# Performance work log

Measured on AMD Instinct MI355X. Metric: run time of the kernel, lower is better.

The kernel has to match this reference:

```python
import jax, jax.numpy as jnp
import numpy as np

N, E, D, L = 50000, 400000, 128, 5
NTYPE, NATTR, NDEPTH = 100, 100, 21
BN_EPS = 1e-5


def _bn(z, gamma, beta):
    # training-mode BatchNorm1d over the node axis (biased variance, as torch)
    mu = jnp.mean(z, axis=0)
    var = jnp.mean(jnp.square(z - mu), axis=0)
    return (z - mu) * jax.lax.rsqrt(var + BN_EPS) * gamma + beta


def setup_inputs() -> dict:
    key = jax.random.key(0)
    ks = jax.random.split(key, 20)
    s = 0.05
    inp = {
        "x": jax.random.randint(ks[0], (N, 2), 0, NTYPE),
        "node_depth": jax.random.randint(ks[1], (N,), 0, NDEPTH),
        "edge_index": jax.random.randint(ks[2], (2, E), 0, N),
        "edge_attr": jax.random.normal(ks[3], (E, 2), dtype=jnp.float32),
        # node encoder tables
        "type_emb": jax.random.normal(ks[4], (NTYPE, D)) * s,
        "attr_emb": jax.random.normal(ks[5], (NATTR, D)) * s,
        "depth_emb": jax.random.normal(ks[6], (NDEPTH, D)) * s,
        # per-layer GIN params, stacked over L
        "We": jax.random.normal(ks[7], (L, 2, D)) * s,
        "be": jnp.zeros((L, D)),
        "eps": jnp.zeros((L,)),
        "W1": jax.random.normal(ks[8], (L, D, 2 * D)) * s,
        "b1": jnp.zeros((L, 2 * D)),
        "g1": jnp.ones((L, 2 * D)),
        "bt1": jnp.zeros((L, 2 * D)),
        "W2": jax.random.normal(ks[9], (L, 2 * D, D)) * s,
        "b2": jnp.zeros((L, D)),
        "go": jnp.ones((L, D)),
        "bo": jnp.zeros((L, D)),
    }
    return inp


def reference(x, node_depth, edge_index, edge_attr,
              type_emb, attr_emb, depth_emb,
              We, be, eps, W1, b1, g1, bt1, W2, b2, go, bo):
    # node encoder: type + attr + depth embeddings  -> [N, D]
    h = (type_emb[x[:, 0]] + attr_emb[x[:, 1]]
         + depth_emb[jnp.clip(node_depth, 0, NDEPTH - 1)])
    src, dst = edge_index[0], edge_index[1]
    n = h.shape[0]
    for l in range(L):
        # GINConv: gather -> relu(x_j + edge_emb) -> scatter-add
        edge_emb = edge_attr @ We[l] + be[l]                 # [E, D]
        msg = jax.nn.relu(h[src] + edge_emb)                 # [E, D]
        agg = jax.ops.segment_sum(msg, dst, num_segments=n)  # [N, D]
        z = (1.0 + eps[l]) * h + agg
        # mlp: Linear -> BN -> ReLU -> Linear
        z = _bn(z @ W1[l] + b1[l], g1[l], bt1[l])
        z = jax.nn.relu(z) @ W2[l] + b2[l]
        # outer batchnorm
        z = _bn(z, go[l], bo[l])
        if l < L - 1:  # relu on all but last layer (dropout p=0 -> identity)
            z = jax.nn.relu(z)
        h = z
    return h  # JK='last'
```

## Files before the change

kernel.cpp:

```cpp
#include <hip/hip_runtime.h>
#include <hip/hip_bf16.h>

#define NN  50000
#define NE  400000
#define DD  128
#define DD2 256
#define NL  5
#define NB_SCAN 196
#define GB  256
#define NCH 1563

typedef __hip_bfloat16 bf16;
typedef __attribute__((ext_vector_type(8))) short bf16x8;
typedef __attribute__((ext_vector_type(4))) float f32x4;

__device__ __forceinline__ float b2f(bf16 v) { return __bfloat162float(v); }
__device__ __forceinline__ bool probe_bf(const void* g1) {
    return ((const unsigned*)g1)[0] == 0x3F803F80u;
}
__device__ __forceinline__ float ldp(const void* p, int i, bool bf) {
    return bf ? b2f(((const bf16*)p)[i]) : ((const float*)p)[i];
}
__device__ __forceinline__ void ldp8(const void* p, int i, bool bf, float* o) {
    if (bf) {
        union { int4 v; bf16 b[8]; } u;
        u.v = *(const int4*)((const bf16*)p + i);
#pragma unroll
        for (int j = 0; j < 8; j++) o[j] = b2f(u.b[j]);
    } else {
        float4 a = *(const float4*)((const float*)p + i);
        float4 b = *(const float4*)((const float*)p + i + 4);
        o[0]=a.x; o[1]=a.y; o[2]=a.z; o[3]=a.w;
        o[4]=b.x; o[5]=b.y; o[6]=b.z; o[7]=b.w;
    }
}

__global__ void enc_kernel(const int* __restrict__ x, const int* __restrict__ dep,
                           const void* te, const void* ae, const void* de,
                           const void* probe, float* __restrict__ h,
                           bf16* __restrict__ h2, int h2ok) {
    int t = blockIdx.x * 256 + threadIdx.x;
    if (t >= NN * DD) return;
    bool bf = probe_bf(probe);
    int i = t >> 7, d = t & (DD - 1);
    int dp = dep[i];
    dp = dp < 0 ? 0 : (dp > 20 ? 20 : dp);
    float a = ldp(te, x[2 * i] * DD + d, bf);
    float b = ldp(ae, x[2 * i + 1] * DD + d, bf);
    float c = ldp(de, dp * DD + d, bf);
    float s;
    if (bf) {
        s = b2f(__float2bfloat16(a + b));
        s = b2f(__float2bfloat16(s + c));
    } else {
        s = a + b + c;
    }
    h[t] = s;
    if (h2ok) h2[t] = __float2bfloat16(s);
}

__global__ void hist_kernel(const int* __restrict__ ei, int* __restrict__ cnt) {
    int e = blockIdx.x * 256 + threadIdx.x;
    if (e < NE) atomicAdd(&cnt[ei[NE + e]], 1);
}

__global__ void bsum_kernel(const int* __restrict__ cnt, int* __restrict__ bsum) {
    __shared__ int sm[256];
    int i = blockIdx.x * 256 + threadIdx.x;
    sm[threadIdx.x] = (i < NN) ? cnt[i] : 0;
    __syncthreads();
    for (int s = 128; s > 0; s >>= 1) {
        if (threadIdx.x < s) sm[threadIdx.x] += sm[threadIdx.x + s];
        __syncthreads();
    }
    if (threadIdx.x == 0) bsum[blockIdx.x] = sm[0];
}

__global__ void bscan_kernel(const int* __restrict__ bsum, int* __restrict__ boff, int nb) {
    __shared__ int sm[256];
    int t = threadIdx.x;
    int v = (t < nb) ? bsum[t] : 0;
    sm[t] = v; __syncthreads();
    for (int s = 1; s < 256; s <<= 1) {
        int a = (t >= s) ? sm[t - s] : 0;
        __syncthreads();
        sm[t] += a;
        __syncthreads();
    }
    if (t < nb) boff[t] = sm[t] - v;
}

__global__ void offs_kernel(const int* __restrict__ cnt, const int* __restrict__ boff,
                            int* __restrict__ offs, int* __restrict__ cur) {
    __shared__ int sm[256];
    int t = threadIdx.x;
    int i = blockIdx.x * 256 + t;
    int v = (i < NN) ? cnt[i] : 0;
    sm[t] = v; __syncthreads();
    for (int s = 1; s < 256; s <<= 1) {
        int a = (t >= s) ? sm[t - s] : 0;
        __syncthreads();
        sm[t] += a;
        __syncthreads();
    }
    int excl = sm[t] - v + boff[blockIdx.x];
    if (i < NN) { offs[i] = excl; cur[i] = excl; }
    if (i == NN - 1) offs[NN] = excl + v;
}

__global__ void place_kernel(const int* __restrict__ ei, const float* __restrict__ ea,
                             int* __restrict__ cur, int* __restrict__ srcS,
                             unsigned* __restrict__ eaS) {
    int e = blockIdx.x * 256 + threadIdx.x;
    if (e >= NE) return;
    int dst = ei[NE + e];
    int p = atomicAdd(&cur[dst], 1);
    srcS[p] = ei[e];
    union { bf16 b[2]; unsigned u; } pk;
    pk.b[0] = __float2bfloat16(ea[2 * e]);
    pk.b[1] = __float2bfloat16(ea[2 * e + 1]);
    eaS[p] = pk.u;
}

__global__ void wtrans2_kernel(const void* W1, const void* W2, const void* probe,
                               bf16* __restrict__ W1tH, bf16* __restrict__ W1tL,
                               bf16* __restrict__ W2tH, bf16* __restrict__ W2tL) {
    bool bf = probe_bf(probe);
    int idx = blockIdx.x * 256 + threadIdx.x;
    if (idx >= NL * DD * DD2) return;
    int l = idx / (DD * DD2), rem = idx % (DD * DD2);
    {
        int k = rem / DD2, n = rem % DD2;
        float w = ldp(W1, idx, bf);
        bf16 hb = __float2bfloat16(w);
        size_t o = ((size_t)l * DD2 + n) * DD + k;
        W1tH[o] = hb;
        W1tL[o] = __float2bfloat16(w - b2f(hb));
    }
    {
        int k = rem / DD, n = rem % DD;
        float w = ldp(W2, idx, bf);
        bf16 hb = __float2bfloat16(w);
        size_t o = ((size_t)l * DD + n) * DD2 + k;
        W2tH[o] = hb;
        W2tL[o] = __float2bfloat16(w - b2f(hb));
    }
}

template<int H2, int FIRST>
__global__ __launch_bounds__(256)
void agg_v3(const int* __restrict__ offs, const int* __restrict__ srcS,
            const unsigned* __restrict__ eaS, const void* We, const void* be,
            const void* epsp, const void* probe, const float* __restrict__ zmid,
            const bf16* __restrict__ zmid2, const float* __restrict__ s2v,
            const float* __restrict__ t2v, float* __restrict__ aggout, int l) {
    bool bf = probe_bf(probe);
    int wave = threadIdx.x >> 6, lane = threadIdx.x & 63;
    int node = blockIdx.x * 4 + wave;
    if (node >= NN) return;
    int d0 = lane * 2;
    float w00 = ldp(We, l * 2 * DD + d0, bf),      w01 = ldp(We, l * 2 * DD + d0 + 1, bf);
    float w10 = ldp(We, l * 2 * DD + DD + d0, bf), w11 = ldp(We, l * 2 * DD + DD + d0 + 1, bf);
    float bb0 = ldp(be, l * DD + d0, bf),          bb1 = ldp(be, l * DD + d0 + 1, bf);
    float cf = 1.0f + ldp(epsp, l, bf);
    float s20 = 1.f, s21 = 1.f, t20 = 0.f, t21 = 0.f;
    if (!FIRST) {
        float2 sv = *(const float2*)&s2v[d0];
        float2 tv = *(const float2*)&t2v[d0];
        s20 = sv.x; s21 = sv.y; t20 = tv.x; t21 = tv.y;
    }
    int s = offs[node], e = offs[node + 1];
    float acc0 = 0.f, acc1 = 0.f;
    int j = s;
#define AGG_ONE(SRC, EA)                                                        \
    {   float hx, hy;                                                          \
        if (H2) { union { unsigned u; bf16 b[2]; } hv;                         \
                  hv.u = *(const unsigned*)&zmid2[(size_t)(SRC) * DD + d0];    \
                  hx = b2f(hv.b[0]); hy = b2f(hv.b[1]); }                      \
        else    { float2 hv = *(const float2*)&zmid[(size_t)(SRC) * DD + d0];  \
                  hx = hv.x; hy = hv.y; }                                      \
        if (!FIRST) {                                                          \
            hx = fmaxf(fmaf(hx, s20, t20), 0.f);                               \
            hy = fmaxf(fmaf(hy, s21, t21), 0.f);                               \
        }                                                                      \
        union { unsigned u; bf16 b[2]; } ap; ap.u = (EA);                      \
        float ax = b2f(ap.b[0]), ay = b2f(ap.b[1]);                            \
        acc0 += fmaxf(hx + ax * w00 + ay * w10 + bb0, 0.f);                    \
        acc1 += fmaxf(hy + ax * w01 + ay * w11 + bb1, 0.f); }
    for (; j + 8 <= e; j += 8) {
        int i0=srcS[j],i1=srcS[j+1],i2=srcS[j+2],i3=srcS[j+3];
        int i4=srcS[j+4],i5=srcS[j+5],i6=srcS[j+6],i7=srcS[j+7];
        unsigned e0=eaS[j],e1=eaS[j+1],e2=eaS[j+2],e3=eaS[j+3];
        unsigned e4=eaS[j+4],e5=eaS[j+5],e6=eaS[j+6],e7=eaS[j+7];
        AGG_ONE(i0,e0) AGG_ONE(i1,e1) AGG_ONE(i2,e2) AGG_ONE(i3,e3)
        AGG_ONE(i4,e4) AGG_ONE(i5,e5) AGG_ONE(i6,e6) AGG_ONE(i7,e7)
    }
    for (; j + 4 <= e; j += 4) {
        int i0=srcS[j],i1=srcS[j+1],i2=srcS[j+2],i3=srcS[j+3];
        unsigned e0=eaS[j],e1=eaS[j+1],e2=eaS[j+2],e3=eaS[j+3];
        AGG_ONE(i0,e0) AGG_ONE(i1,e1) AGG_ONE(i2,e2) AGG_ONE(i3,e3)
    }
    for (; j < e; j++) { int i0 = srcS[j]; unsigned e0 = eaS[j]; AGG_ONE(i0,e0) }
#undef AGG_ONE
    float2 zs = *(const float2*)&zmid[(size_t)node * DD + d0];
    float h0 = zs.x, h1 = zs.y;
    if (!FIRST) {
        h0 = fmaxf(fmaf(h0, s20, t20), 0.f);
        h1 = fmaxf(fmaf(h1, s21, t21), 0.f);
    }
    float2 o; o.x = fmaf(cf, h0, acc0); o.y = fmaf(cf, h1, acc1);
    *(float2*)&aggout[(size_t)node * DD + d0] = o;
}

__global__ __launch_bounds__(512, 2)
void gemm1_v2(const float* __restrict__ zpre, const bf16* __restrict__ W1tH,
              const bf16* __restrict__ W1tL, const void* b1, const void* probe,
              bf16* __restrict__ z1, float* __restrict__ P1s, float* __restrict__ P1q,
              int l) {
    __shared__ float smS[DD2], smQ[DD2];
    bool bf = probe_bf(probe);
    int tid = threadIdx.x;
    int lane = tid & 63, wave = tid >> 6;
    int wq = wave & 3, wr = wave >> 2;
    int ln15 = lane & 15, kg = lane >> 4;

    const bf16* WlH = W1tH + (size_t)l * DD2 * DD;
    const bf16* WlL = W1tL + (size_t)l * DD2 * DD;

    bf16x8 bh[4][4], bl[4][4];
#pragma unroll
    for (int t = 0; t < 4; t++) {
        int n = (wq * 4 + t) * 16 + ln15;
#pragma unroll
        for (int s = 0; s < 4; s++) {
            size_t off = (size_t)n * DD + s * 32 + kg * 8;
            bh[t][s] = *(const bf16x8*)&WlH[off];
            bl[t][s] = *(const bf16x8*)&WlL[off];
        }
    }
    float bias[4];
#pragma unroll
    for (int t = 0; t < 4; t++) bias[t] = ldp(b1, l * DD2 + (wq * 4 + t) * 16 + ln15, bf);

    float sp[4] = {0.f, 0.f, 0.f, 0.f}, qp[4] = {0.f, 0.f, 0.f, 0.f};

    for (int chunk = blockIdx.x; chunk < NCH; chunk += GB) {
        int rowbase = chunk * 32 + wr * 16;
        int arow = rowbase + ln15;
        bool aval = arow < NN;
        f32x4 acc[4];
#pragma unroll
        for (int t = 0; t < 4; t++) acc[t] = (f32x4){0.f, 0.f, 0.f, 0.f};
#pragma unroll
        for (int s = 0; s < 4; s++) {
            float av[8];
            if (aval) {
                float4 p0 = *(const float4*)&zpre[(size_t)arow * DD + s * 32 + kg * 8];
                float4 p1 = *(const float4*)&zpre[(size_t)arow * DD + s * 32 + kg * 8 + 4];
                av[0]=p0.x; av[1]=p0.y; av[2]=p0.z; av[3]=p0.w;
                av[4]=p1.x; av[5]=p1.y; av[6]=p1.z; av[7]=p1.w;
            } else {
#pragma unroll
                for (int j = 0; j < 8; j++) av[j] = 0.f;
            }
            union { bf16x8 v; bf16 e[8]; } ahi, alo;
#pragma unroll
            for (int j = 0; j < 8; j++) {
                bf16 hb = __float2bfloat16(av[j]);
                ahi.e[j] = hb;
                alo.e[j] = __float2bfloat16(av[j] - b2f(hb));
            }
#pragma unroll
            for (int t = 0; t < 4; t++) {
                acc[t] = __builtin_amdgcn_mfma_f32_16x16x32_bf16(ahi.v, bh[t][s], acc[t], 0, 0, 0);
                acc[t] = __builtin_amdgcn_mfma_f32_16x16x32_bf16(alo.v, bh[t][s], acc[t], 0, 0, 0);
                acc[t] = __builtin_amdgcn_mfma_f32_16x16x32_bf16(ahi.v, bl[t][s], acc[t], 0, 0, 0);
            }
        }
#pragma unroll
        for (int t = 0; t < 4; t++) {
            int col = (wq * 4 + t) * 16 + ln15;
#pragma unroll
            for (int r = 0; r < 4; r++) {
                int row = rowbase + kg * 4 + r;
                if (row < NN) {
                    float zv = acc[t][r] + bias[t];
                    bf16 zb = __float2bfloat16(zv);
                    z1[(size_t)row * DD2 + col] = zb;
                    float vv = b2f(zb);
                    sp[t] += vv; qp[t] += vv * vv;
                }
            }
        }
    }
#pragma unroll
    for (int t = 0; t < 4; t++) {
        sp[t] += __shfl_xor(sp[t], 16); sp[t] += __shfl_xor(sp[t], 32);
        qp[t] += __shfl_xor(qp[t], 16); qp[t] += __shfl_xor(qp[t], 32);
    }
    if (tid < DD2) { smS[tid] = 0.f; smQ[tid] = 0.f; }
    __syncthreads();
    if ((lane & 48) == 0) {
#pragma unroll
        for (int t = 0; t < 4; t++) {
            int col = (wq * 4 + t) * 16 + ln15;
            atomicAdd(&smS[col], sp[t]);
            atomicAdd(&smQ[col], qp[t]);
        }
    }
    __syncthreads();
    if (tid < DD2) {
        P1s[(size_t)blockIdx.x * DD2 + tid] = smS[tid];
        P1q[(size_t)blockIdx.x * DD2 + tid] = smQ[tid];
    }
}

__global__ __launch_bounds__(512, 2)
void gemm2_v2(const bf16* __restrict__ z1, const float* __restrict__ s1,
              const float* __restrict__ t1, const bf16* __restrict__ W2tH,
              const bf16* __restrict__ W2tL, const void* b2, const void* probe,
              float* __restrict__ out, bf16* __restrict__ out2, int shadow,
              float* __restrict__ P2s, float* __restrict__ P2q, int l) {
    __shared__ float smS[DD], smQ[DD];
    bool bf = probe_bf(probe);
    int tid = threadIdx.x;
    int lane = tid & 63, wave = tid >> 6;
    int wq = wave & 3, wr = wave >> 2;
    int ln15 = lane & 15, kg = lane >> 4;

    const bf16* WlH = W2tH + (size_t)l * DD * DD2;
    const bf16* WlL = W2tL + (size_t)l * DD * DD2;

    bf16x8 bh[2][8], bl[2][8];
#pragma unroll
    for (int t = 0; t < 2; t++) {
        int n = (wq * 2 + t) * 16 + ln15;
#pragma unroll
        for (int s = 0; s < 8; s++) {
            size_t off = (size_t)n * DD2 + s * 32 + kg * 8;
            bh[t][s] = *(const bf16x8*)&WlH[off];
            bl[t][s] = *(const bf16x8*)&WlL[off];
        }
    }
    float bias[2];
#pragma unroll
    for (int t = 0; t < 2; t++) bias[t] = ldp(b2, l * DD + (wq * 2 + t) * 16 + ln15, bf);

    float sp[2] = {0.f, 0.f}, qp[2] = {0.f, 0.f};

    for (int chunk = blockIdx.x; chunk < NCH; chunk += GB) {
        int rowbase = chunk * 32 + wr * 16;
        int arow = rowbase + ln15;
        bool aval = arow < NN;
        f32x4 acc[2];
        acc[0] = (f32x4){0.f, 0.f, 0.f, 0.f};
        acc[1] = (f32x4){0.f, 0.f, 0.f, 0.f};
#pragma unroll
        for (int s = 0; s < 8; s++) {
            int k0 = s * 32 + kg * 8;
            float az[8];
            if (aval) {
                union { int4 v; bf16 b[8]; } u;
                u.v = *(const int4*)&z1[(size_t)arow * DD2 + k0];
                float4 c0 = *(const float4*)&s1[k0];
                float4 c1 = *(const float4*)&s1[k0 + 4];
                float4 d0 = *(const float4*)&t1[k0];
                float4 d1 = *(const float4*)&t1[k0 + 4];
                float sc[8] = {c0.x,c0.y,c0.z,c0.w,c1.x,c1.y,c1.z,c1.w};
                float tt[8] = {d0.x,d0.y,d0.z,d0.w,d1.x,d1.y,d1.z,d1.w};
#pragma unroll
                for (int j = 0; j < 8; j++)
                    az[j] = fmaxf(fmaf(b2f(u.b[j]), sc[j], tt[j]), 0.f);
            } else {
#pragma unroll
                for (int j = 0; j < 8; j++) az[j] = 0.f;
            }
            union { bf16x8 v; bf16 e[8]; } ahi, alo;
#pragma unroll
            for (int j = 0; j < 8; j++) {
                bf16 hb = __float2bfloat16(az[j]);
                ahi.e[j] = hb;
                alo.e[j] = __float2bfloat16(az[j] - b2f(hb));
            }
#pragma unroll
            for (int t = 0; t < 2; t++) {
                acc[t] = __builtin_amdgcn_mfma_f32_16x16x32_bf16(ahi.v, bh[t][s], acc[t], 0, 0, 0);
                acc[t] = __builtin_amdgcn_mfma_f32_16x16x32_bf16(alo.v, bh[t][s], acc[t], 0, 0, 0);
                acc[t] = __builtin_amdgcn_mfma_f32_16x16x32_bf16(ahi.v, bl[t][s], acc[t], 0, 0, 0);
            }
        }
#pragma unroll
        for (int t = 0; t < 2; t++) {
            int col = (wq * 2 + t) * 16 + ln15;
#pragma unroll
            for (int r = 0; r < 4; r++) {
                int row = rowbase + kg * 4 + r;
                if (row < NN) {
                    float zv = acc[t][r] + bias[t];
                    out[(size_t)row * DD + col] = zv;
                    if (shadow) out2[(size_t)row * DD + col] = __float2bfloat16(zv);
                    sp[t] += zv; qp[t] += zv * zv;
                }
            }
        }
    }
#pragma unroll
    for (int t = 0; t < 2; t++) {
        sp[t] += __shfl_xor(sp[t], 16); sp[t] += __shfl_xor(sp[t], 32);
        qp[t] += __shfl_xor(qp[t], 16); qp[t] += __shfl_xor(qp[t], 32);
    }
    if (tid < DD) { smS[tid] = 0.f; smQ[tid] = 0.f; }
    __syncthreads();
    if ((lane & 48) == 0) {
#pragma unroll
        for (int t = 0; t < 2; t++) {
            int col = (wq * 2 + t) * 16 + ln15;
            atomicAdd(&smS[col], sp[t]);
            atomicAdd(&smQ[col], qp[t]);
        }
    }
    __syncthreads();
    if (tid < DD) {
        P2s[(size_t)blockIdx.x * DD + tid] = smS[tid];
        P2q[(size_t)blockIdx.x * DD + tid] = smQ[tid];
    }
}

template<int C>
__global__ void fin_v3(const float* __restrict__ Ps, const float* __restrict__ Pq,
                       const void* gamma, const void* beta, const void* probe,
                       float* __restrict__ s, float* __restrict__ t, int l) {
    __shared__ float rs[256], rq[256];
    int c = blockIdx.x;
    int b = threadIdx.x;
    rs[b] = Ps[(size_t)b * C + c];
    rq[b] = Pq[(size_t)b * C + c];
    __syncthreads();
    for (int k = 128; k > 0; k >>= 1) {
        if (b < k) { rs[b] += rs[b + k]; rq[b] += rq[b + k]; }
        __syncthreads();
    }
    if (b == 0) {
        bool bf = probe_bf(probe);
        const float inv = 1.0f / (float)NN;
        float mu = rs[0] * inv;
        float var = rq[0] * inv - mu * mu;
        float sc = ldp(gamma, l * C + c, bf) * rsqrtf(var + 1e-5f);
        s[c] = sc;
        t[c] = ldp(beta, l * C + c, bf) - mu * sc;
    }
}

__global__ void bn_apply2(const float* __restrict__ zin, const float* __restrict__ s,
                          const float* __restrict__ t, float* __restrict__ out,
                          bf16* __restrict__ h2, int relu, int h2ok) {
    int i = blockIdx.x * 256 + threadIdx.x;
    if (i >= NN * DD / 4) return;
    int d = (i * 4) & (DD - 1);
    float4 v = ((const float4*)zin)[i];
    float4 sc = *(const float4*)&s[d];
    float4 tt = *(const float4*)&t[d];
    float4 r;
    r.x = fmaf(v.x, sc.x, tt.x);
    r.y = fmaf(v.y, sc.y, tt.y);
    r.z = fmaf(v.z, sc.z, tt.z);
    r.w = fmaf(v.w, sc.w, tt.w);
    if (relu) {
        r.x = fmaxf(r.x, 0.f); r.y = fmaxf(r.y, 0.f);
        r.z = fmaxf(r.z, 0.f); r.w = fmaxf(r.w, 0.f);
    }
    ((float4*)out)[i] = r;
    if (h2ok) {
        union { bf16 b[4]; int2 p; } o;
        o.b[0] = __float2bfloat16(r.x); o.b[1] = __float2bfloat16(r.y);
        o.b[2] = __float2bfloat16(r.z); o.b[3] = __float2bfloat16(r.w);
        *(int2*)&h2[(size_t)i * 4] = o.p;
    }
}

__global__ void scatter_kernel(const int* __restrict__ ei, const float* __restrict__ ea,
                               const void* We, const void* be, const void* probe,
                               const float* __restrict__ h, float* __restrict__ agg,
                               int l, int aok) {
    if (!aok) return;
    bool bf = probe_bf(probe);
    int e = blockIdx.x * 2 + (threadIdx.x >> 7);
    int d = threadIdx.x & (DD - 1);
    int src = ei[e];
    int dst = ei[NE + e];
    float a0 = ea[2 * e], a1 = ea[2 * e + 1];
    float w0 = ldp(We, l * 2 * DD + d, bf);
    float w1 = ldp(We, l * 2 * DD + DD + d, bf);
    float bb = ldp(be, l * DD + d, bf);
    float m = h[src * DD + d] + a0 * w0 + a1 * w1 + bb;
    if (m > 0.0f) atomicAdd(&agg[dst * DD + d], m);
}

__global__ __launch_bounds__(256)
void gemm1_kernel(const float* __restrict__ zin, const float* __restrict__ h,
                  const void* W1, const void* b1, const void* epsp, const void* probe,
                  bf16* __restrict__ z1, int l, int zok) {
    __shared__ float zs[32][36];
    __shared__ float wsh[32][DD2];
    bool bf = probe_bf(probe);
    int tid = threadIdx.x;
    int tx = tid & 31, ty = tid >> 5;
    int row0 = blockIdx.x * 32;
    if (row0 >= NN) return;
    float cf = 1.0f + ldp(epsp, l, bf);
    float acc[4][8];
#pragma unroll
    for (int i = 0; i < 4; i++)
#pragma unroll
        for (int j = 0; j < 8; j++) acc[i][j] = 0.0f;
    int lrow = tid >> 3, lkc = (tid & 7) * 4, wkr = tid >> 5, wcol = (tid & 31) * 8;
    for (int k0 = 0; k0 < DD; k0 += 32) {
        int gr = row0 + lrow;
        float4 zv = make_float4(0.f, 0.f, 0.f, 0.f);
        if (gr < NN) {
            zv = *(const float4*)&zin[gr * DD + k0 + lkc];
            float4 hv = *(const float4*)&h[gr * DD + k0 + lkc];
            zv.x = fmaf(cf, hv.x, zv.x); zv.y = fmaf(cf, hv.y, zv.y);
            zv.z = fmaf(cf, hv.z, zv.z); zv.w = fmaf(cf, hv.w, zv.w);
        }
        *(float4*)&zs[lrow][lkc] = zv;
#pragma unroll
        for (int m = 0; m < 4; m++) {
            int kr = wkr + m * 8;
            float wv[8];
            ldp8(W1, l * DD * DD2 + (k0 + kr) * DD2 + wcol, bf, wv);
            *(float4*)&wsh[kr][wcol]     = make_float4(wv[0], wv[1], wv[2], wv[3]);
            *(float4*)&wsh[kr][wcol + 4] = make_float4(wv[4], wv[5], wv[6], wv[7]);
        }
        __syncthreads();
#pragma unroll 4
        for (int kk = 0; kk < 32; kk++) {
            float zr[4];
#pragma unroll
            for (int i = 0; i < 4; i++) zr[i] = zs[ty * 4 + i][kk];
            float4 w0 = *(float4*)&wsh[kk][tx * 8];
            float4 w1 = *(float4*)&wsh[kk][tx * 8 + 4];
            float wv[8] = {w0.x, w0.y, w0.z, w0.w, w1.x, w1.y, w1.z, w1.w};
#pragma unroll
            for (int i = 0; i < 4; i++)
#pragma unroll
                for (int j = 0; j < 8; j++)
                    acc[i][j] = fmaf(zr[i], wv[j], acc[i][j]);
        }
        __syncthreads();
    }
    float bv[8];
    ldp8(b1, l * DD2 + tx * 8, bf, bv);
#pragma unroll
    for (int i = 0; i < 4; i++) {
        int gr = row0 + ty * 4 + i;
        if (gr < NN && zok) {
            union { int4 v; bf16 b[8]; } o;
#pragma unroll
            for (int j = 0; j < 8; j++) o.b[j] = __float2bfloat16(acc[i][j] + bv[j]);
            *(int4*)&z1[(long)gr * DD2 + tx * 8] = o.v;
        }
    }
}

__global__ __launch_bounds__(256)
void gemm2_kernel(const bf16* __restrict__ z1, const float* __restrict__ s1,
                  const float* __restrict__ t1, const void* W2, const void* b2,
                  const void* probe, float* __restrict__ out, int l, int aok, int zok) {
    __shared__ float zs[32][36];
    __shared__ float wsh[32][DD];
    bool bf = probe_bf(probe);
    int tid = threadIdx.x;
    int tx = tid & 15, ty = tid >> 4;
    int row0 = blockIdx.x * 32;
    if (row0 >= NN) return;
    float acc[2][8];
#pragma unroll
    for (int i = 0; i < 2; i++)
#pragma unroll
        for (int j = 0; j < 8; j++) acc[i][j] = 0.0f;
    int lrow = tid >> 3, lkc = (tid & 7) * 4, wkr = tid >> 4, wcol = (tid & 15) * 8;
    for (int k0 = 0; k0 < DD2; k0 += 32) {
        int gr = row0 + lrow;
        float4 zv = make_float4(0.f, 0.f, 0.f, 0.f);
        if (gr < NN && zok) {
            union { int2 v; bf16 b[4]; } u;
            u.v = *(const int2*)&z1[(long)gr * DD2 + k0 + lkc];
            float4 sc = *(const float4*)&s1[k0 + lkc];
            float4 tt = *(const float4*)&t1[k0 + lkc];
            zv.x = fmaxf(0.f, fmaf(b2f(u.b[0]), sc.x, tt.x));
            zv.y = fmaxf(0.f, fmaf(b2f(u.b[1]), sc.y, tt.y));
            zv.z = fmaxf(0.f, fmaf(b2f(u.b[2]), sc.z, tt.z));
            zv.w = fmaxf(0.f, fmaf(b2f(u.b[3]), sc.w, tt.w));
        }
        *(float4*)&zs[lrow][lkc] = zv;
#pragma unroll
        for (int m = 0; m < 2; m++) {
            int kr = wkr + m * 16;
            float wv[8];
            ldp8(W2, l * DD2 * DD + (k0 + kr) * DD + wcol, bf, wv);
            *(float4*)&wsh[kr][wcol]     = make_float4(wv[0], wv[1], wv[2], wv[3]);
            *(float4*)&wsh[kr][wcol + 4] = make_float4(wv[4], wv[5], wv[6], wv[7]);
        }
        __syncthreads();
#pragma unroll 4
        for (int kk = 0; kk < 32; kk++) {
            float zr[2];
            zr[0] = zs[ty * 2][kk];
            zr[1] = zs[ty * 2 + 1][kk];
            float4 w0 = *(float4*)&wsh[kk][tx * 8];
            float4 w1 = *(float4*)&wsh[kk][tx * 8 + 4];
            float wv[8] = {w0.x, w0.y, w0.z, w0.w, w1.x, w1.y, w1.z, w1.w};
#pragma unroll
            for (int i = 0; i < 2; i++)
#pragma unroll
                for (int j = 0; j < 8; j++)
                    acc[i][j] = fmaf(zr[i], wv[j], acc[i][j]);
        }
        __syncthreads();
    }
    float bv[8];
    ldp8(b2, l * DD + tx * 8, bf, bv);
#pragma unroll
    for (int i = 0; i < 2; i++) {
        int gr = row0 + ty * 2 + i;
        if (gr < NN && aok) {
            float4 o0 = make_float4(acc[i][0] + bv[0], acc[i][1] + bv[1],
                                    acc[i][2] + bv[2], acc[i][3] + bv[3]);
            float4 o1 = make_float4(acc[i][4] + bv[4], acc[i][5] + bv[5],
                                    acc[i][6] + bv[6], acc[i][7] + bv[7]);
            *(float4*)&out[gr * DD + tx * 8] = o0;
            *(float4*)&out[gr * DD + tx * 8 + 4] = o1;
        }
    }
}

__global__ void bn_stats1_kernel(const bf16* __restrict__ z, float* __restrict__ sum,
                                 float* __restrict__ sq, int zok) {
    int col = threadIdx.x;
    int rbase = blockIdx.x * 256;
    int rend = rbase + 256; if (rend > NN) rend = NN;
    float s = 0.0f, q = 0.0f;
    if (zok)
        for (int r = rbase; r < rend; r++) {
            float v = b2f(z[(long)r * DD2 + col]);
            s += v; q += v * v;
        }
    atomicAdd(&sum[col], s);
    atomicAdd(&sq[col], q);
}

__global__ void bn_stats2_kernel(const float* __restrict__ z, float* __restrict__ sum,
                                 float* __restrict__ sq, int aok) {
    int col = threadIdx.x & (DD - 1);
    int roff = threadIdx.x >> 7;
    int rbase = blockIdx.x * 256;
    int rend = rbase + 256; if (rend > NN) rend = NN;
    float s = 0.0f, q = 0.0f;
    if (aok)
        for (int r = rbase + roff; r < rend; r += 2) {
            float v = z[(long)r * DD + col];
            s += v; q += v * v;
        }
    atomicAdd(&sum[col], s);
    atomicAdd(&sq[col], q);
}

template<int C>
__global__ void bn_finalize_kernel(const float* __restrict__ sum, const float* __restrict__ sq,
                                   const void* gamma, const void* beta, const void* probe,
                                   float* __restrict__ s, float* __restrict__ t, int l) {
    int c = threadIdx.x;
    if (c >= C) return;
    bool bf = probe_bf(probe);
    const float inv = 1.0f / (float)NN;
    float mu = sum[c] * inv;
    float var = sq[c] * inv - mu * mu;
    float sc = ldp(gamma, l * C + c, bf) * rsqrtf(var + 1e-5f);
    s[c] = sc;
    t[c] = ldp(beta, l * C + c, bf) - mu * sc;
}

extern "C" void kernel_launch(void* const* d_in, const int* in_sizes, int n_in,
                              void* d_out, int out_size, void* d_ws, size_t ws_size,
                              hipStream_t stream) {
    const int*   x   = (const int*)d_in[0];
    const int*   dep = (const int*)d_in[1];
    const int*   ei  = (const int*)d_in[2];
    const float* ea  = (const float*)d_in[3];
    const void* te  = d_in[4];
    const void* ae  = d_in[5];
    const void* de  = d_in[6];
    const void* We  = d_in[7];
    const void* be  = d_in[8];
    const void* eps = d_in[9];
    const void* W1  = d_in[10];
    const void* b1  = d_in[11];
    const void* g1  = d_in[12];
    const void* bt1 = d_in[13];
    const void* W2  = d_in[14];
    const void* b2  = d_in[15];
    const void* go  = d_in[16];
    const void* bo  = d_in[17];

    float* zmid = (float*)d_out;
    float* ws = (float*)d_ws;
    float* sum1 = ws;
    float* sq1  = ws + 256;
    float* sum2 = ws + 512;
    float* sq2  = ws + 640;
    float* s1   = ws + 768;
    float* t1   = ws + 1024;
    float* s2   = ws + 1280;
    float* t2   = ws + 1408;

    float*  P1s  = ws + 2048;
    float*  P1q  = P1s + GB * DD2;
    float*  P2s  = P1q + GB * DD2;
    float*  P2q  = P2s + GB * DD;
    int*    cnt  = (int*)(P2q + GB * DD);
    int*    offs = cnt + 50048;
    int*    cur  = offs + 50048;
    int*    bsum = cur + 50048;
    int*    boff = bsum + 256;
    int*    srcS = boff + 256;
    unsigned* eaS = (unsigned*)(srcS + NE);
    float*  aggout = (float*)(eaS + NE);
    bf16*   z1S   = (bf16*)(aggout + (size_t)NN * DD);
    bf16*   W1tH  = z1S + (size_t)NN * DD2;
    bf16*   W1tL  = W1tH + (size_t)NL * DD2 * DD;
    bf16*   W2tH  = W1tL + (size_t)NL * DD2 * DD;
    bf16*   W2tL  = W2tH + (size_t)NL * DD * DD2;
    bf16*   zmid2 = W2tL + (size_t)NL * DD * DD2;
    size_t need_noh2 = (size_t)((char*)zmid2 - (char*)d_ws);
    size_t need_full = need_noh2 + (size_t)NN * DD * sizeof(bf16);

    float* zpreF = ws + 2048;
    bf16*  z1F   = (bf16*)(zpreF + (size_t)NN * DD);
    size_t need_a = 2048u * 4 + (size_t)NN * DD * 4;
    size_t need_z = need_a + (size_t)NN * DD2 * 2;

    int mode = ws_size >= need_full ? 2 : (ws_size >= need_noh2 ? 1 : 0);
    int aok = mode || ws_size >= need_a ? 1 : 0;
    int zok = mode || ws_size >= need_z ? 1 : 0;
    bf16* z1 = mode ? z1S : z1F;

    enc_kernel<<<(NN * DD + 255) / 256, 256, 0, stream>>>(x, dep, te, ae, de, g1, zmid, zmid2, mode == 2);

    if (mode) {
        hipMemsetAsync(cnt, 0, 50048 * sizeof(int), stream);
        hist_kernel<<<(NE + 255) / 256, 256, 0, stream>>>(ei, cnt);
        bsum_kernel<<<NB_SCAN, 256, 0, stream>>>(cnt, bsum);
        bscan_kernel<<<1, 256, 0, stream>>>(bsum, boff, NB_SCAN);
        offs_kernel<<<NB_SCAN, 256, 0, stream>>>(cnt, boff, offs, cur);
        place_kernel<<<(NE + 255) / 256, 256, 0, stream>>>(ei, ea, cur, srcS, eaS);
        wtrans2_kernel<<<(NL * DD * DD2 + 255) / 256, 256, 0, stream>>>(W1, W2, g1, W1tH, W1tL, W2tH, W2tL);
    }

    for (int l = 0; l < NL; l++) {
        if (mode) {
            if (mode == 2) {
                if (l == 0)
                    agg_v3<1,1><<<(NN + 3) / 4, 256, 0, stream>>>(offs, srcS, eaS, We, be, eps, g1,
                                                                  zmid, zmid2, s2, t2, aggout, l);
                else
                    agg_v3<1,0><<<(NN + 3) / 4, 256, 0, stream>>>(offs, srcS, eaS, We, be, eps, g1,
                                                                  zmid, zmid2, s2, t2, aggout, l);
            } else {
                if (l == 0)
                    agg_v3<0,1><<<(NN + 3) / 4, 256, 0, stream>>>(offs, srcS, eaS, We, be, eps, g1,
                                                                  zmid, zmid2, s2, t2, aggout, l);
                else
                    agg_v3<0,0><<<(NN + 3) / 4, 256, 0, stream>>>(offs, srcS, eaS, We, be, eps, g1,
                                                                  zmid, zmid2, s2, t2, aggout, l);
            }
            gemm1_v2<<<GB, 512, 0, stream>>>(aggout, W1tH, W1tL, b1, g1, z1, P1s, P1q, l);
            fin_v3<DD2><<<DD2, 256, 0, stream>>>(P1s, P1q, g1, bt1, g1, s1, t1, l);
            gemm2_v2<<<GB, 512, 0, stream>>>(z1, s1, t1, W2tH, W2tL, b2, g1, zmid, zmid2,
                                             (mode == 2 && l < NL - 1) ? 1 : 0, P2s, P2q, l);
            fin_v3<DD><<<DD, 256, 0, stream>>>(P2s, P2q, go, bo, g1, s2, t2, l);
        } else {
            hipMemsetAsync(ws, 0, 768 * sizeof(float), stream);
            if (aok) hipMemsetAsync(zpreF, 0, (size_t)NN * DD * sizeof(float), stream);
            scatter_kernel<<<NE / 2, 256, 0, stream>>>(ei, ea, We, be, g1, zmid, zpreF, l, aok);
            gemm1_kernel<<<(NN + 31) / 32, 256, 0, stream>>>(zpreF, zmid, W1, b1, eps, g1, z1, l, zok);
            bn_stats1_kernel<<<(NN + 255) / 256, 256, 0, stream>>>(z1, sum1, sq1, zok);
            bn_finalize_kernel<DD2><<<1, DD2, 0, stream>>>(sum1, sq1, g1, bt1, g1, s1, t1, l);
            gemm2_kernel<<<(NN + 31) / 32, 256, 0, stream>>>(z1, s1, t1, W2, b2, g1, zpreF, l, aok, zok);
            bn_stats2_kernel<<<(NN + 255) / 256, 256, 0, stream>>>(zpreF, sum2, sq2, aok);
            bn_finalize_kernel<DD><<<1, DD, 0, stream>>>(sum2, sq2, go, bo, g1, s2, t2, l);
            bn_apply2<<<(NN * DD / 4 + 255) / 256, 256, 0, stream>>>(
                zpreF, s2, t2, zmid, zmid2, l < NL - 1 ? 1 : 0, 0);
        }
    }
    if (mode)
        bn_apply2<<<(NN * DD / 4 + 255) / 256, 256, 0, stream>>>(zmid, s2, t2, zmid, zmid2, 0, 0);
}
```

Before: 642.9 us.

## Retile gemm1 to 16-row chunks per block and double GEMM grid sizes

gemm1 is restructured so each block handles 16-row chunks, with each of its 8 waves owning 32 output columns. This halves the weight fragments held in registers and drops the bounds checks, since 50000 divides evenly by 16. Both GEMMs now launch 512 blocks with launch_bounds occupancy raised to 4, and the BN finalize kernel loops over a variable number of partial blocks. The goal is more waves in flight to hide memory latency, at the cost of more partial-statistic rows to reduce and register pressure that could cause spills at the higher occupancy bound.

```diff
diff --git a/kernel.cpp b/kernel.cpp
--- a/kernel.cpp
+++ b/kernel.cpp
@@ -7,8 +7,10 @@
 #define DD2 256
 #define NL  5
 #define NB_SCAN 196
-#define GB  256
-#define NCH 1563
+#define GB1 512
+#define GB2 512
+#define NCH1 3125
+#define NCH2 1563
 
 typedef __hip_bfloat16 bf16;
 typedef __attribute__((ext_vector_type(8))) short bf16x8;
@@ -212,8 +214,8 @@
     *(float2*)&aggout[(size_t)node * DD + d0] = o;
 }
 
-__global__ __launch_bounds__(512, 2)
-void gemm1_v2(const float* __restrict__ zpre, const bf16* __restrict__ W1tH,
+__global__ __launch_bounds__(512, 4)
+void gemm1_v3(const float* __restrict__ zpre, const bf16* __restrict__ W1tH,
               const bf16* __restrict__ W1tL, const void* b1, const void* probe,
               bf16* __restrict__ z1, float* __restrict__ P1s, float* __restrict__ P1q,
               int l) {
@@ -221,16 +223,15 @@
     bool bf = probe_bf(probe);
     int tid = threadIdx.x;
     int lane = tid & 63, wave = tid >> 6;
-    int wq = wave & 3, wr = wave >> 2;
     int ln15 = lane & 15, kg = lane >> 4;
 
     const bf16* WlH = W1tH + (size_t)l * DD2 * DD;
     const bf16* WlL = W1tL + (size_t)l * DD2 * DD;
 
-    bf16x8 bh[4][4], bl[4][4];
-#pragma unroll
-    for (int t = 0; t < 4; t++) {
-        int n = (wq * 4 + t) * 16 + ln15;
+    bf16x8 bh[2][4], bl[2][4];
+#pragma unroll
+    for (int t = 0; t < 2; t++) {
+        int n = (wave * 2 + t) * 16 + ln15;
 #pragma unroll
         for (int s = 0; s < 4; s++) {
             size_t off = (size_t)n * DD + s * 32 + kg * 8;
@@ -238,31 +239,23 @@
             bl[t][s] = *(const bf16x8*)&WlL[off];
         }
     }
-    float bias[4];
-#pragma unroll
-    for (int t = 0; t < 4; t++) bias[t] = ldp(b1, l * DD2 + (wq * 4 + t) * 16 + ln15, bf);
-
-    float sp[4] = {0.f, 0.f, 0.f, 0.f}, qp[4] = {0.f, 0.f, 0.f, 0.f};
-
-    for (int chunk = blockIdx.x; chunk < NCH; chunk += GB) {
-        int rowbase = chunk * 32 + wr * 16;
+    float bias[2];
+#pragma unroll
+    for (int t = 0; t < 2; t++) bias[t] = ldp(b1, l * DD2 + (wave * 2 + t) * 16 + ln15, bf);
+
+    float sp[2] = {0.f, 0.f}, qp[2] = {0.f, 0.f};
+
+    for (int chunk = blockIdx.x; chunk < NCH1; chunk += GB1) {
+        int rowbase = chunk * 16;
         int arow = rowbase + ln15;
-        bool aval = arow < NN;
-        f32x4 acc[4];
-#pragma unroll
-        for (int t = 0; t < 4; t++) acc[t] = (f32x4){0.f, 0.f, 0.f, 0.f};
+        f32x4 acc[2];
+        acc[0] = (f32x4){0.f, 0.f, 0.f, 0.f};
+        acc[1] = (f32x4){0.f, 0.f, 0.f, 0.f};
 #pragma unroll
         for (int s = 0; s < 4; s++) {
-            float av[8];
-            if (aval) {
-                float4 p0 = *(const float4*)&zpre[(size_t)arow * DD + s * 32 + kg * 8];
-                float4 p1 = *(const float4*)&zpre[(size_t)arow * DD + s * 32 + kg * 8 + 4];
-                av[0]=p0.x; av[1]=p0.y; av[2]=p0.z; av[3]=p0.w;
-                av[4]=p1.x; av[5]=p1.y; av[6]=p1.z; av[7]=p1.w;
-            } else {
-#pragma unroll
-                for (int j = 0; j < 8; j++) av[j] = 0.f;
-            }
+            float4 p0 = *(const float4*)&zpre[(size_t)arow * DD + s * 32 + kg * 8];
+            float4 p1 = *(const float4*)&zpre[(size_t)arow * DD + s * 32 + kg * 8 + 4];
+            float av[8] = {p0.x, p0.y, p0.z, p0.w, p1.x, p1.y, p1.z, p1.w};
             union { bf16x8 v; bf16 e[8]; } ahi, alo;
 #pragma unroll
             for (int j = 0; j < 8; j++) {
@@ -271,30 +264,28 @@
                 alo.e[j] = __float2bfloat16(av[j] - b2f(hb));
             }
 #pragma unroll
-            for (int t = 0; t < 4; t++) {
+            for (int t = 0; t < 2; t++) {
                 acc[t] = __builtin_amdgcn_mfma_f32_16x16x32_bf16(ahi.v, bh[t][s], acc[t], 0, 0, 0);
                 acc[t] = __builtin_amdgcn_mfma_f32_16x16x32_bf16(alo.v, bh[t][s], acc[t], 0, 0, 0);
                 acc[t] = __builtin_amdgcn_mfma_f32_16x16x32_bf16(ahi.v, bl[t][s], acc[t], 0, 0, 0);
             }
         }
 #pragma unroll
-        for (int t = 0; t < 4; t++) {
-            int col = (wq * 4 + t) * 16 + ln15;
+        for (int t = 0; t < 2; t++) {
+            int col = (wave * 2 + t) * 16 + ln15;
 #pragma unroll
             for (int r = 0; r < 4; r++) {
                 int row = rowbase + kg * 4 + r;
-                if (row < NN) {
-                    float zv = acc[t][r] + bias[t];
-                    bf16 zb = __float2bfloat16(zv);
-                    z1[(size_t)row * DD2 + col] = zb;
-                    float vv = b2f(zb);
-                    sp[t] += vv; qp[t] += vv * vv;
-                }
+                float zv = acc[t][r] + bias[t];
+                bf16 zb = __float2bfloat16(zv);
+                z1[(size_t)row * DD2 + col] = zb;
+                float vv = b2f(zb);
+                sp[t] += vv; qp[t] += vv * vv;
             }
         }
     }
 #pragma unroll
-    for (int t = 0; t < 4; t++) {
+    for (int t = 0; t < 2; t++) {
         sp[t] += __shfl_xor(sp[t], 16); sp[t] += __shfl_xor(sp[t], 32);
         qp[t] += __shfl_xor(qp[t], 16); qp[t] += __shfl_xor(qp[t], 32);
     }
@@ -302,10 +293,10 @@
     __syncthreads();
     if ((lane & 48) == 0) {
 #pragma unroll
-        for (int t = 0; t < 4; t++) {
-            int col = (wq * 4 + t) * 16 + ln15;
-            atomicAdd(&smS[col], sp[t]);
-            atomicAdd(&smQ[col], qp[t]);
+        for (int t = 0; t < 2; t++) {
+            int col = (wave * 2 + t) * 16 + ln15;
+            smS[col] = sp[t];
+            smQ[col] = qp[t];
         }
     }
     __syncthreads();
@@ -315,7 +306,7 @@
     }
 }
 
-__global__ __launch_bounds__(512, 2)
+__global__ __launch_bounds__(512, 4)
 void gemm2_v2(const bf16* __restrict__ z1, const float* __restrict__ s1,
               const float* __restrict__ t1, const bf16* __restrict__ W2tH,
               const bf16* __restrict__ W2tL, const void* b2, const void* probe,
@@ -348,7 +339,7 @@
 
     float sp[2] = {0.f, 0.f}, qp[2] = {0.f, 0.f};
 
-    for (int chunk = blockIdx.x; chunk < NCH; chunk += GB) {
+    for (int chunk = blockIdx.x; chunk < NCH2; chunk += GB2) {
         int rowbase = chunk * 32 + wr * 16;
         int arow = rowbase + ln15;
         bool aval = arow < NN;
@@ -428,19 +419,22 @@
 
 template<int C>
 __global__ void fin_v3(const float* __restrict__ Ps, const float* __restrict__ Pq,
-                       const void* gamma, const void* beta, const void* probe,
+                       int nb, const void* gamma, const void* beta, const void* probe,
                        float* __restrict__ s, float* __restrict__ t, int l) {
     __shared__ float rs[256], rq[256];
     int c = blockIdx.x;
-    int b = threadIdx.x;
-    rs[b] = Ps[(size_t)b * C + c];
-    rq[b] = Pq[(size_t)b * C + c];
+    float ss = 0.f, qq = 0.f;
+    for (int b = threadIdx.x; b < nb; b += 256) {
+        ss += Ps[(size_t)b * C + c];
+        qq += Pq[(size_t)b * C + c];
+    }
+    rs[threadIdx.x] = ss; rq[threadIdx.x] = qq;
     __syncthreads();
     for (int k = 128; k > 0; k >>= 1) {
-        if (b < k) { rs[b] += rs[b + k]; rq[b] += rq[b + k]; }
-        __syncthreads();
-    }
-    if (b == 0) {
+        if (threadIdx.x < k) { rs[threadIdx.x] += rs[threadIdx.x + k]; rq[threadIdx.x] += rq[threadIdx.x + k]; }
+        __syncthreads();
+    }
+    if (threadIdx.x == 0) {
         bool bf = probe_bf(probe);
         const float inv = 1.0f / (float)NN;
         float mu = rs[0] * inv;
@@ -715,10 +709,10 @@
     float* t2   = ws + 1408;
 
     float*  P1s  = ws + 2048;
-    float*  P1q  = P1s + GB * DD2;
-    float*  P2s  = P1q + GB * DD2;
-    float*  P2q  = P2s + GB * DD;
-    int*    cnt  = (int*)(P2q + GB * DD);
+    float*  P1q  = P1s + (size_t)GB1 * DD2;
+    float*  P2s  = P1q + (size_t)GB1 * DD2;
+    float*  P2q  = P2s + (size_t)GB2 * DD;
+    int*    cnt  = (int*)(P2q + (size_t)GB2 * DD);
     int*    offs = cnt + 50048;
     int*    cur  = offs + 50048;
     int*    bsum = cur + 50048;
@@ -774,11 +768,11 @@
                     agg_v3<0,0><<<(NN + 3) / 4, 256, 0, stream>>>(offs, srcS, eaS, We, be, eps, g1,
                                                                   zmid, zmid2, s2, t2, aggout, l);
             }
-            gemm1_v2<<<GB, 512, 0, stream>>>(aggout, W1tH, W1tL, b1, g1, z1, P1s, P1q, l);
-            fin_v3<DD2><<<DD2, 256, 0, stream>>>(P1s, P1q, g1, bt1, g1, s1, t1, l);
-            gemm2_v2<<<GB, 512, 0, stream>>>(z1, s1, t1, W2tH, W2tL, b2, g1, zmid, zmid2,
-                                             (mode == 2 && l < NL - 1) ? 1 : 0, P2s, P2q, l);
-            fin_v3<DD><<<DD, 256, 0, stream>>>(P2s, P2q, go, bo, g1, s2, t2, l);
+            gemm1_v3<<<GB1, 512, 0, stream>>>(aggout, W1tH, W1tL, b1, g1, z1, P1s, P1q, l);
+            fin_v3<DD2><<<DD2, 256, 0, stream>>>(P1s, P1q, GB1, g1, bt1, g1, s1, t1, l);
+            gemm2_v2<<<GB2, 512, 0, stream>>>(z1, s1, t1, W2tH, W2tL, b2, g1, zmid, zmid2,
+                                              (mode == 2 && l < NL - 1) ? 1 : 0, P2s, P2q, l);
+            fin_v3<DD><<<DD, 256, 0, stream>>>(P2s, P2q, GB2, go, bo, g1, s2, t2, l);
         } else {
             hipMemsetAsync(ws, 0, 768 * sizeof(float), stream);
             if (aok) hipMemsetAsync(zpreF, 0, (size_t)NN * DD * sizeof(float), stream);
```

Result: slower. 815.8 us (+26.9%).
